# Optimization experiments

Measured on AMD Instinct MI355X. Metric: run time of the kernel, lower is better.

The kernel has to match this reference:

```python
import jax, jax.numpy as jnp
import numpy as np

EPS = 1e-8

def setup_inputs() -> dict:
    key = jax.random.key(0)
    k1, k2, k3 = jax.random.split(key, 3)
    B, N, L = 4096, 8192, 256
    logits = jax.random.normal(k1, (B, N), dtype=jnp.float32)
    positive_ids = jax.random.randint(k2, (B, L), 0, N, dtype=jnp.int64)
    positive_weights = jax.random.uniform(k3, (B, L), dtype=jnp.float32)
    return {"logits": logits, "positive_ids": positive_ids, "positive_weights": positive_weights}

def reference(logits, positive_ids, positive_weights):
    # gather positive logits: [B, L]
    gathered = jnp.take_along_axis(logits, positive_ids, axis=1)
    w = positive_weights.astype(jnp.float32)
    w = w / jnp.maximum(w.sum(axis=-1, keepdims=True), EPS)
    # sort by weight descending
    order = jnp.argsort(-w, axis=-1)
    ordered_logits = jnp.take_along_axis(gathered, order, axis=1)
    ordered_weights = jnp.take_along_axis(w, order, axis=1)
    # suffix logsumexp in one reverse cumulative pass: [B, L]
    suffix_lse = jax.lax.cumlogsumexp(ordered_logits, axis=1, reverse=True)
    listmle = jnp.sum(ordered_weights * (suffix_lse - ordered_logits), axis=-1)
    return jnp.mean(listmle)
```

## Files before the change

kernel.cpp:

```cpp
#include <hip/hip_runtime.h>
#include <hip/hip_bf16.h>
#include <math.h>

#define BROWS 4096
#define NCOLS 8192
#define LLEN  256
#define EPSV  1e-8f

__global__ __launch_bounds__(256) void listmle_kernel(
    const float* __restrict__ logits,
    const int*   __restrict__ ids,
    const float* __restrict__ weights,
    float*       __restrict__ partial)
{
    __shared__ float    s_g[LLEN];
    __shared__ float    s_w[LLEN];
    __shared__ unsigned s_key[2][LLEN];
    __shared__ float    s_aggm[4], s_aggs[4];
    __shared__ float    s_redt[4], s_redw[4];

    const int tid  = threadIdx.x;
    const int lane = tid & 63;
    const int wv   = tid >> 6;
    const int b    = blockIdx.x;

    float w  = weights[(size_t)b * LLEN + tid];
    int   id = ids[(size_t)b * LLEN + tid];
    float g  = logits[(size_t)b * NCOLS + id];

    unsigned key = (__float_as_uint(w) & 0xFFFFFF00u) | (unsigned)(LLEN - 1 - tid);

    #pragma unroll
    for (int k = 2; k <= 64; k <<= 1) {
        #pragma unroll
        for (int j = k >> 1; j > 0; j >>= 1) {
            const bool keep_max = (((tid & k) == 0) == ((tid & j) == 0));
            unsigned p  = __shfl_xor(key, j);
            unsigned mx = key > p ? key : p;
            unsigned mn = key > p ? p : key;
            key = keep_max ? mx : mn;
        }
    }

    s_g[tid] = g;
    s_w[tid] = w;

    int phase = 0;
    #pragma unroll
    for (int k = 128; k <= LLEN; k <<= 1) {
        #pragma unroll
        for (int j = k >> 1; j > 0; j >>= 1) {
            const bool keep_max = (((tid & k) == 0) == ((tid & j) == 0));
            unsigned p;
            if (j >= 64) {
                s_key[phase][tid] = key;
                __syncthreads();
                p = s_key[phase][tid ^ j];
                phase ^= 1;
            } else {
                p = __shfl_xor(key, j);
            }
            unsigned mx = key > p ? key : p;
            unsigned mn = key > p ? p : key;
            key = keep_max ? mx : mn;
        }
    }

    const int pos = (LLEN - 1) - (int)(key & 0xFFu);
    float og = s_g[pos];
    float ow = s_w[pos];

    float m = og, s = 1.0f;
    #pragma unroll
    for (int off = 1; off < 64; off <<= 1) {
        float mp = __shfl_down(m, off);
        float sp = __shfl_down(s, off);
        if (lane + off < 64) {
            float nm = fmaxf(m, mp);
            s = s * __expf(m - nm) + sp * __expf(mp - nm);
            m = nm;
        }
    }
    if (lane == 0) { s_aggm[wv] = m; s_aggs[wv] = s; }
    __syncthreads();
    #pragma unroll
    for (int w2 = 0; w2 < 4; ++w2) {
        if (w2 > wv) {
            float mp = s_aggm[w2], sp = s_aggs[w2];
            float nm = fmaxf(m, mp);
            s = s * __expf(m - nm) + sp * __expf(mp - nm);
            m = nm;
        }
    }
    float suffix_lse = m + __logf(s);

    float t  = ow * (suffix_lse - og);
    float ws = ow;
    #pragma unroll
    for (int o = 32; o > 0; o >>= 1) {
        t  += __shfl_down(t, o);
        ws += __shfl_down(ws, o);
    }
    if (lane == 0) { s_redt[wv] = t; s_redw[wv] = ws; }
    __syncthreads();
    if (tid == 0) {
        float tot  = s_redt[0] + s_redt[1] + s_redt[2] + s_redt[3];
        float wsum = s_redw[0] + s_redw[1] + s_redw[2] + s_redw[3];
        partial[b] = tot / fmaxf(wsum, EPSV);
    }
}

__global__ __launch_bounds__(256) void reduce_kernel(
    const float* __restrict__ partial, float* __restrict__ out)
{
    __shared__ float s_red[4];
    const int tid  = threadIdx.x;
    const int lane = tid & 63;
    const int wv   = tid >> 6;

    float v = 0.0f;
    #pragma unroll
    for (int i = 0; i < BROWS / 256; ++i)
        v += partial[i * 256 + tid];

    #pragma unroll
    for (int o = 32; o > 0; o >>= 1) v += __shfl_down(v, o);
    if (lane == 0) s_red[wv] = v;
    __syncthreads();
    if (tid == 0)
        out[0] = (s_red[0] + s_red[1] + s_red[2] + s_red[3]) * (1.0f / (float)BROWS);
}

extern "C" void kernel_launch(void* const* d_in, const int* in_sizes, int n_in,
                              void* d_out, int out_size, void* d_ws, size_t ws_size,
                              hipStream_t stream) {
    const float* logits  = (const float*)d_in[0];
    const int*   ids     = (const int*)d_in[1];
    const float* weights = (const float*)d_in[2];
    float* out     = (float*)d_out;
    float* partial = (float*)d_ws;

    listmle_kernel<<<dim3(BROWS), dim3(LLEN), 0, stream>>>(logits, ids, weights, partial);
    reduce_kernel<<<dim3(1), dim3(256), 0, stream>>>(partial, out);
}
```

Measured before the change: 188.6 us.

## Stream full logits row into LDS via async DMA and fuse final reduction

Instead of gathering 256 scattered logits per row from global memory, each block asynchronously copies its entire 8192-float row into shared memory with global_load_lds, overlapping the copy with the weight sort, then gathers from LDS. The separate reduce kernel is replaced by a last-block-done pattern using an atomic counter, with a memset to reset it. This trades random global accesses for a fully coalesced read of the whole logits matrix and 32KB of LDS per block, which may reduce occupancy.

```diff
diff --git a/kernel.cpp b/kernel.cpp
--- a/kernel.cpp
+++ b/kernel.cpp
@@ -7,26 +7,45 @@
 #define LLEN  256
 #define EPSV  1e-8f
 
+__device__ __forceinline__ void lse_combine(float& m, float& s, float mo, float so) {
+    float nm = fmaxf(m, mo);
+    s = s * __expf(m - nm) + so * __expf(mo - nm);
+    m = nm;
+}
+
 __global__ __launch_bounds__(256) void listmle_kernel(
     const float* __restrict__ logits,
     const int*   __restrict__ ids,
     const float* __restrict__ weights,
-    float*       __restrict__ partial)
+    float*       __restrict__ partial,
+    unsigned*    __restrict__ counter,
+    float*       __restrict__ out)
 {
-    __shared__ float    s_g[LLEN];
+    __shared__ float    s_row[NCOLS];
     __shared__ float    s_w[LLEN];
+    __shared__ int      s_id[LLEN];
     __shared__ unsigned s_key[2][LLEN];
     __shared__ float    s_aggm[4], s_aggs[4];
     __shared__ float    s_redt[4], s_redw[4];
+    __shared__ int      s_last;
 
     const int tid  = threadIdx.x;
     const int lane = tid & 63;
     const int wv   = tid >> 6;
     const int b    = blockIdx.x;
 
+    const float* row = logits + (size_t)b * NCOLS;
+    #pragma unroll
+    for (int it = 0; it < 8; ++it) {
+        const int off = wv * 2048 + it * 256;
+        __builtin_amdgcn_global_load_lds(
+            (const __attribute__((address_space(1))) void*)(row + off + lane * 4),
+            (__attribute__((address_space(3))) void*)(s_row + off),
+            16, 0, 0);
+    }
+
     float w  = weights[(size_t)b * LLEN + tid];
     int   id = ids[(size_t)b * LLEN + tid];
-    float g  = logits[(size_t)b * NCOLS + id];
 
     unsigned key = (__float_as_uint(w) & 0xFFFFFF00u) | (unsigned)(LLEN - 1 - tid);
 
@@ -42,8 +61,8 @@
         }
     }
 
-    s_g[tid] = g;
-    s_w[tid] = w;
+    s_w[tid]  = w;
+    s_id[tid] = id;
 
     int phase = 0;
     #pragma unroll
@@ -67,30 +86,21 @@
     }
 
     const int pos = (LLEN - 1) - (int)(key & 0xFFu);
-    float og = s_g[pos];
-    float ow = s_w[pos];
+    const float ow = s_w[pos];
+    const float og = s_row[s_id[pos]];
 
     float m = og, s = 1.0f;
     #pragma unroll
     for (int off = 1; off < 64; off <<= 1) {
         float mp = __shfl_down(m, off);
         float sp = __shfl_down(s, off);
-        if (lane + off < 64) {
-            float nm = fmaxf(m, mp);
-            s = s * __expf(m - nm) + sp * __expf(mp - nm);
-            m = nm;
-        }
+        if (lane + off < 64) lse_combine(m, s, mp, sp);
     }
     if (lane == 0) { s_aggm[wv] = m; s_aggs[wv] = s; }
     __syncthreads();
     #pragma unroll
     for (int w2 = 0; w2 < 4; ++w2) {
-        if (w2 > wv) {
-            float mp = s_aggm[w2], sp = s_aggs[w2];
-            float nm = fmaxf(m, mp);
-            s = s * __expf(m - nm) + sp * __expf(mp - nm);
-            m = nm;
-        }
+        if (w2 > wv) lse_combine(m, s, s_aggm[w2], s_aggs[w2]);
     }
     float suffix_lse = m + __logf(s);
 
@@ -107,28 +117,27 @@
         float tot  = s_redt[0] + s_redt[1] + s_redt[2] + s_redt[3];
         float wsum = s_redw[0] + s_redw[1] + s_redw[2] + s_redw[3];
         partial[b] = tot / fmaxf(wsum, EPSV);
+        __threadfence();
+        unsigned old = atomicAdd(counter, 1u);
+        s_last = (old == BROWS - 1) ? 1 : 0;
     }
-}
+    __syncthreads();
 
-__global__ __launch_bounds__(256) void reduce_kernel(
-    const float* __restrict__ partial, float* __restrict__ out)
-{
-    __shared__ float s_red[4];
-    const int tid  = threadIdx.x;
-    const int lane = tid & 63;
-    const int wv   = tid >> 6;
-
-    float v = 0.0f;
-    #pragma unroll
-    for (int i = 0; i < BROWS / 256; ++i)
-        v += partial[i * 256 + tid];
-
-    #pragma unroll
-    for (int o = 32; o > 0; o >>= 1) v += __shfl_down(v, o);
-    if (lane == 0) s_red[wv] = v;
-    __syncthreads();
-    if (tid == 0)
-        out[0] = (s_red[0] + s_red[1] + s_red[2] + s_red[3]) * (1.0f / (float)BROWS);
+    if (s_last) {
+        __threadfence();
+        float v = 0.0f;
+        #pragma unroll
+        for (int i = 0; i < BROWS / 256; ++i)
+            v += __hip_atomic_load(&partial[i * 256 + tid],
+                                   __ATOMIC_RELAXED, __HIP_MEMORY_SCOPE_AGENT);
+        #pragma unroll
+        for (int o = 32; o > 0; o >>= 1) v += __shfl_down(v, o);
+        if (lane == 0) s_redt[wv] = v;
+        __syncthreads();
+        if (tid == 0)
+            out[0] = (s_redt[0] + s_redt[1] + s_redt[2] + s_redt[3])
+                   * (1.0f / (float)BROWS);
+    }
 }
 
 extern "C" void kernel_launch(void* const* d_in, const int* in_sizes, int n_in,
@@ -137,9 +146,11 @@
     const float* logits  = (const float*)d_in[0];
     const int*   ids     = (const int*)d_in[1];
     const float* weights = (const float*)d_in[2];
-    float* out     = (float*)d_out;
-    float* partial = (float*)d_ws;
+    float*    out     = (float*)d_out;
+    float*    partial = (float*)d_ws;
+    unsigned* counter = (unsigned*)d_ws + BROWS;
 
-    listmle_kernel<<<dim3(BROWS), dim3(LLEN), 0, stream>>>(logits, ids, weights, partial);
-    reduce_kernel<<<dim3(1), dim3(256), 0, stream>>>(partial, out);
+    hipMemsetAsync(counter, 0, sizeof(unsigned), stream);
+    listmle_kernel<<<dim3(BROWS), dim3(LLEN), 0, stream>>>(
+        logits, ids, weights, partial, counter, out);
 }
```

After: 373.9 us. 98.2% more time.
